# Performance work log

Hardware: AMD Instinct MI355X
Metric: run time of the kernel (lower is better)

## Reference

```python
import jax, jax.numpy as jnp
import numpy as np

B, S, D = 16, 2048, 256

def setup_inputs() -> dict:
    key = jax.random.key(0)
    ks = jax.random.split(key, 7)
    scale = 1.0 / np.sqrt(D)
    return {
        "x": jax.random.normal(ks[0], (B, S, D), dtype=jnp.float32),
        "Wq": jax.random.normal(ks[1], (D, D), dtype=jnp.float32) * scale,
        "bq": jax.random.normal(ks[2], (D,), dtype=jnp.float32) * 0.01,
        "Wk": jax.random.normal(ks[3], (D, D), dtype=jnp.float32) * scale,
        "bk": jax.random.normal(ks[4], (D,), dtype=jnp.float32) * 0.01,
        "Wv": jax.random.normal(ks[5], (D, D), dtype=jnp.float32) * scale,
        "bv": jax.random.normal(ks[6], (D,), dtype=jnp.float32) * 0.01,
    }

def reference(x, Wq, bq, Wk, bk, Wv, bv):
    # q,k,v: [B,S,D]
    q = x @ Wq + bq
    k = x @ Wk + bk
    v = x @ Wv + bv
    inv_sqrt_d = jnp.asarray(1.0 / np.sqrt(x.shape[-1]), dtype=x.dtype)
    energy = jnp.einsum('bqd,bkd->bqk', q, k) * inv_sqrt_d  # [B,S,S]
    attn = jax.nn.softmax(energy, axis=-1)
    weighted = jnp.einsum('bqk,bkd->bqd', attn, v)  # [B,S,D]
    return weighted.sum(axis=1)  # [B,D]
```

## Files before the change

kernel.cpp:

```cpp
#include <hip/hip_runtime.h>
#include <hip/hip_bf16.h>

typedef __bf16 bf16_t;
typedef bf16_t bf16x8 __attribute__((ext_vector_type(8)));
typedef float  f32x4  __attribute__((ext_vector_type(4)));

constexpr int S = 2048, D = 256;


__device__ __forceinline__ float fast_exp2(float x) {
    return __builtin_amdgcn_exp2f(x);
}

__global__ void wt_kernel(const float* __restrict__ Wq, const float* __restrict__ Wk,
                          const float* __restrict__ Wv, bf16_t* __restrict__ wtf) {
    int idx = blockIdx.x * 256 + threadIdx.x;
    int w    = idx >> 13;
    int rem  = idx & 8191;
    int nt   = rem >> 9;
    int rem2 = rem & 511;
    int ks   = rem2 >> 6;
    int lane = rem2 & 63;
    int lm = lane & 15, lg = lane >> 4;
    const float* Wsrc = (w == 0) ? Wq : (w == 1) ? Wk : Wv;
    int col = nt * 16 + lm, krow = ks * 32 + lg * 8;
    bf16x8 o;
#pragma unroll
    for (int j = 0; j < 8; j++) o[j] = (bf16_t)Wsrc[(krow + j) * 256 + col];
    *(bf16x8*)(wtf + (size_t)idx * 8) = o;
}

__global__ __launch_bounds__(256) void proj_kernel(
    const float* __restrict__ x, const bf16_t* __restrict__ wtf,
    const float* __restrict__ bq, const float* __restrict__ bk, const float* __restrict__ bv,
    bf16_t* __restrict__ qo, bf16_t* __restrict__ ko, bf16_t* __restrict__ vo) {
    __shared__ float xs[2][128 * 36];
    int w    = blockIdx.y;
    int tid  = threadIdx.x;
    int wave = tid >> 6, lane = tid & 63, lm = lane & 15, lg = lane >> 4;
    int m0   = blockIdx.x * 128;
    const bf16_t* wb   = wtf + w * 65536;
    const float*  bias = (w == 0) ? bq : (w == 1) ? bk : bv;

    f32x4 acc[2][16];
#pragma unroll
    for (int s = 0; s < 2; s++)
#pragma unroll
        for (int nt = 0; nt < 16; nt++) acc[s][nt] = f32x4{0.f, 0.f, 0.f, 0.f};

    float4 stg[4];
#pragma unroll
    for (int u = 0; u < 4; u++) {
        int f = u * 256 + tid, row = f >> 3, c4 = f & 7;
        stg[u] = *(const float4*)(x + (size_t)(m0 + row) * 256 + c4 * 4);
    }

    for (int ks = 0; ks < 8; ks++) {
        int p = ks & 1;
#pragma unroll
        for (int u = 0; u < 4; u++) {
            int f = u * 256 + tid, row = f >> 3, c4 = f & 7;
            *(float4*)&xs[p][row * 36 + c4 * 4] = stg[u];
        }
        if (ks < 7) {
#pragma unroll
            for (int u = 0; u < 4; u++) {
                int f = u * 256 + tid, row = f >> 3, c4 = f & 7;
                stg[u] = *(const float4*)(x + (size_t)(m0 + row) * 256 + (ks + 1) * 32 + c4 * 4);
            }
        }
        __syncthreads();
        bf16x8 af[2];
#pragma unroll
        for (int s = 0; s < 2; s++) {
            const float* sp = &xs[p][(wave * 32 + s * 16 + lm) * 36 + lg * 8];
            float4 h0 = *(const float4*)sp;
            float4 h1 = *(const float4*)(sp + 4);
            af[s][0] = (bf16_t)h0.x; af[s][1] = (bf16_t)h0.y;
            af[s][2] = (bf16_t)h0.z; af[s][3] = (bf16_t)h0.w;
            af[s][4] = (bf16_t)h1.x; af[s][5] = (bf16_t)h1.y;
            af[s][6] = (bf16_t)h1.z; af[s][7] = (bf16_t)h1.w;
        }
#pragma unroll
        for (int nt = 0; nt < 16; nt++) {
            bf16x8 bfr = *(const bf16x8*)(wb + (size_t)(nt * 8 + ks) * 512 + lane * 8);
            acc[0][nt] = __builtin_amdgcn_mfma_f32_16x16x32_bf16(af[0], bfr, acc[0][nt], 0, 0, 0);
            acc[1][nt] = __builtin_amdgcn_mfma_f32_16x16x32_bf16(af[1], bfr, acc[1][nt], 0, 0, 0);
        }
    }

    __syncthreads();
    bf16_t* sb = ((bf16_t*)&xs[0][0]) + wave * 4480;
    int bglob = m0 >> 11;
#pragma unroll
    for (int s = 0; s < 2; s++) {
#pragma unroll
        for (int nt = 0; nt < 16; nt++) {
            int col = nt * 16 + lm;
            float bval = bias[col];
#pragma unroll
            for (int r = 0; r < 4; r++)
                sb[(lg * 4 + r) * 280 + col] = (bf16_t)(acc[s][nt][r] + bval);
        }
        if (w == 2) {
            int ssrow = (m0 & 2047) + wave * 32 + s * 16 + lm;
#pragma unroll
            for (int ks = 0; ks < 8; ks++) {
                bf16x8 v8 = *(const bf16x8*)&sb[lm * 280 + ks * 32 + lg * 8];
                *(bf16x8*)(vo + ((size_t)(bglob * 2048 + ssrow)) * 256 + ks * 32 + lg * 8) = v8;
            }
        } else {
            bf16_t* dst = (w == 0) ? qo : ko;
            int qb = ((m0 & 2047) >> 4) + wave * 2 + s;
#pragma unroll
            for (int ks = 0; ks < 8; ks++) {
                bf16x8 v8 = *(const bf16x8*)&sb[lm * 280 + ks * 32 + lg * 8];
                *(bf16x8*)(dst + ((size_t)((bglob * 128 + qb) * 8 + ks)) * 512 + lane * 8) = v8;
            }
        }
    }
}

template <int PASS>
__global__ __launch_bounds__(512) void attn_pass(
    const bf16_t* __restrict__ q, const bf16_t* __restrict__ kmat,
    float* __restrict__ lpart, float* __restrict__ wpart) {
    __shared__ bf16_t kst[2][8192];
    __shared__ float  wacc[8][512];

    int tid  = threadIdx.x;
    int wave = tid >> 6, lane = tid & 63, lm = lane & 15, lg = lane >> 4;
    int i  = blockIdx.x;
    int b  = ((i & 7) << 1) | ((i >> 8) & 1);
    int qt = (i >> 3) & 7;
    int kh = (i >> 6) & 3;

    bf16x8 af[2][8];
#pragma unroll
    for (int s = 0; s < 2; s++) {
        const bf16_t* qb = q + ((size_t)((b * 128 + qt * 16 + wave * 2 + s) * 8)) * 512;
#pragma unroll
        for (int ks = 0; ks < 8; ks++)
            af[s][ks] = *(const bf16x8*)(qb + ks * 512 + lane * 8);
    }

    float rinv[2][4];
    if (PASS == 2) {
#pragma unroll
        for (int s = 0; s < 2; s++)
#pragma unroll
            for (int r = 0; r < 4; r++) {
                int row = qt * 256 + wave * 32 + s * 16 + lg * 4 + r;
                float l = 0.f;
#pragma unroll
                for (int k2 = 0; k2 < 4; k2++)
                    l += lpart[(size_t)(k2 * 16 + b) * 2048 + row];
                rinv[s][r] = 1.0f / l;
            }
    }

    float lsum[2][4];
#pragma unroll
    for (int s = 0; s < 2; s++)
#pragma unroll
        for (int r = 0; r < 4; r++) lsum[s][r] = 0.f;

    constexpr float SCL = 0.0625f * 1.44269504f;
    const bf16_t* kb_base = kmat + (size_t)(b * 128 + kh * 32) * 4096;

    bf16x8 stg[2];
#pragma unroll
    for (int u = 0; u < 2; u++)
        stg[u] = *(const bf16x8*)(kb_base + (size_t)(u * 512 + tid) * 8);

    for (int t = 0; t < 16; t++) {
        int p = t & 1;
#pragma unroll
        for (int u = 0; u < 2; u++)
            *(bf16x8*)&kst[p][(u * 512 + tid) * 8] = stg[u];
        if (t < 15) {
#pragma unroll
            for (int u = 0; u < 2; u++)
                stg[u] = *(const bf16x8*)(kb_base + (size_t)(t + 1) * 8192 + (u * 512 + tid) * 8);
        }
        __syncthreads();

        f32x4 sacc[2][2];
#pragma unroll
        for (int s = 0; s < 2; s++)
#pragma unroll
            for (int kb = 0; kb < 2; kb++) sacc[s][kb] = f32x4{0.f, 0.f, 0.f, 0.f};
#pragma unroll
        for (int ks = 0; ks < 8; ks++) {
#pragma unroll
            for (int kb = 0; kb < 2; kb++) {
                bf16x8 bfr = *(const bf16x8*)&kst[p][(kb * 8 + ks) * 512 + lane * 8];
                sacc[0][kb] = __builtin_amdgcn_mfma_f32_16x16x32_bf16(af[0][ks], bfr, sacc[0][kb], 0, 0, 0);
                sacc[1][kb] = __builtin_amdgcn_mfma_f32_16x16x32_bf16(af[1][ks], bfr, sacc[1][kb], 0, 0, 0);
            }
        }

        if (PASS == 1) {
#pragma unroll
            for (int s = 0; s < 2; s++)
#pragma unroll
                for (int kb = 0; kb < 2; kb++)
#pragma unroll
                    for (int r = 0; r < 4; r++)
                        lsum[s][r] += fast_exp2(sacc[s][kb][r] * SCL);
        } else {
            float wv[2] = {0.f, 0.f};
#pragma unroll
            for (int s = 0; s < 2; s++)
#pragma unroll
                for (int kb = 0; kb < 2; kb++)
#pragma unroll
                    for (int r = 0; r < 4; r++)
                        wv[kb] += fast_exp2(sacc[s][kb][r] * SCL) * rinv[s][r];
#pragma unroll
            for (int kb = 0; kb < 2; kb++) {
                float vsum = wv[kb];
                vsum += __shfl_xor(vsum, 16);
                vsum += __shfl_xor(vsum, 32);
                if (lg == 0) wacc[wave][t * 32 + kb * 16 + lm] = vsum;
            }
        }
    }

    if (PASS == 1) {
#pragma unroll
        for (int s = 0; s < 2; s++)
#pragma unroll
            for (int r = 0; r < 4; r++) {
                float v2 = lsum[s][r];
                v2 += __shfl_xor(v2, 1);
                v2 += __shfl_xor(v2, 2);
                v2 += __shfl_xor(v2, 4);
                v2 += __shfl_xor(v2, 8);
                if (lm == 0) {
                    int row = qt * 256 + wave * 32 + s * 16 + lg * 4 + r;
                    lpart[(size_t)(kh * 16 + b) * 2048 + row] = v2;
                }
            }
    } else {
        __syncthreads();
        float sum = 0.f;
#pragma unroll
        for (int w2 = 0; w2 < 8; w2++) sum += wacc[w2][tid];
        wpart[(size_t)(qt * 16 + b) * 2048 + kh * 512 + tid] = sum;
    }
}

__global__ __launch_bounds__(256) void gemv_kernel(
    const float* __restrict__ wpart, const bf16_t* __restrict__ v,
    float* __restrict__ gpart) {
    __shared__ float ldsw[256];
    int b = blockIdx.x >> 3, kseg = blockIdx.x & 7, tid = threadIdx.x;
    int key = kseg * 256 + tid;
    float s = 0.f;
#pragma unroll
    for (int qt = 0; qt < 8; qt++) s += wpart[(size_t)(qt * 16 + b) * 2048 + key];
    ldsw[tid] = s;
    __syncthreads();
    const bf16_t* vb = v + ((size_t)b * 2048 + kseg * 256) * 256;
    float acc = 0.f;
#pragma unroll 4
    for (int t = 0; t < 256; t++) acc += ldsw[t] * (float)vb[(size_t)t * 256 + tid];
    gpart[(size_t)(kseg * 16 + b) * 256 + tid] = acc;
}

__global__ void reduce_kernel(const float* __restrict__ gpart, float* __restrict__ out) {
    int b = blockIdx.x, d = threadIdx.x;
    float t = 0.f;
#pragma unroll
    for (int ks = 0; ks < 8; ks++) t += gpart[(size_t)(ks * 16 + b) * 256 + d];
    out[b * 256 + d] = t;
}

extern "C" void kernel_launch(void* const* d_in, const int* in_sizes, int n_in,
                              void* d_out, int out_size, void* d_ws, size_t ws_size,
                              hipStream_t stream) {
    const float* x  = (const float*)d_in[0];
    const float* Wq = (const float*)d_in[1];
    const float* bq = (const float*)d_in[2];
    const float* Wk = (const float*)d_in[3];
    const float* bk = (const float*)d_in[4];
    const float* Wv = (const float*)d_in[5];
    const float* bv = (const float*)d_in[6];
    float* out = (float*)d_out;

    char* ws = (char*)d_ws;
    bf16_t* wtf   = (bf16_t*)(ws);
    bf16_t* q     = (bf16_t*)(ws + 393216);
    bf16_t* kmat  = (bf16_t*)(ws + 17170432);
    bf16_t* v     = (bf16_t*)(ws + 33947648);
    float*  lpart = (float*) (ws + 50724864);
    float*  wpart = (float*) (ws + 51249152);
    float*  gpart = (float*) (ws + 52297728);

    wt_kernel<<<dim3(96), dim3(256), 0, stream>>>(Wq, Wk, Wv, wtf);
    proj_kernel<<<dim3(256, 3), dim3(256), 0, stream>>>(x, wtf, bq, bk, bv, q, kmat, v);
    attn_pass<1><<<dim3(512), dim3(512), 0, stream>>>(q, kmat, lpart, wpart);
    attn_pass<2><<<dim3(512), dim3(512), 0, stream>>>(q, kmat, lpart, wpart);
    gemv_kernel<<<dim3(128), dim3(256), 0, stream>>>(wpart, v, gpart);
    reduce_kernel<<<dim3(16), dim3(256), 0, stream>>>(gpart, out);
}
```

Baseline: 221.7 us.

## Skip V projection via associativity, reading x directly and enlarging K tiles

The V projection is eliminated by computing the attention-weighted sum of x rows per batch, then applying Wv once to that vector and adding 2048 times bv, since the softmax rows sum to one. This removes a third of the projection GEMM and the bf16 V buffer write and read. The projection kernel now loads x straight from global memory into registers instead of double-buffering through LDS with barriers. The attention kernels process 64 keys per step instead of 32 and store per-wave partials in bf16, which adds LDS use and some rounding error.

```diff
diff --git a/kernel.cpp b/kernel.cpp
--- a/kernel.cpp
+++ b/kernel.cpp
@@ -13,7 +13,7 @@
 }
 
 __global__ void wt_kernel(const float* __restrict__ Wq, const float* __restrict__ Wk,
-                          const float* __restrict__ Wv, bf16_t* __restrict__ wtf) {
+                          bf16_t* __restrict__ wtf) {
     int idx = blockIdx.x * 256 + threadIdx.x;
     int w    = idx >> 13;
     int rem  = idx & 8191;
@@ -22,7 +22,7 @@
     int ks   = rem2 >> 6;
     int lane = rem2 & 63;
     int lm = lane & 15, lg = lane >> 4;
-    const float* Wsrc = (w == 0) ? Wq : (w == 1) ? Wk : Wv;
+    const float* Wsrc = (w == 0) ? Wq : Wk;
     int col = nt * 16 + lm, krow = ks * 32 + lg * 8;
     bf16x8 o;
 #pragma unroll
@@ -32,15 +32,15 @@
 
 __global__ __launch_bounds__(256) void proj_kernel(
     const float* __restrict__ x, const bf16_t* __restrict__ wtf,
-    const float* __restrict__ bq, const float* __restrict__ bk, const float* __restrict__ bv,
-    bf16_t* __restrict__ qo, bf16_t* __restrict__ ko, bf16_t* __restrict__ vo) {
-    __shared__ float xs[2][128 * 36];
+    const float* __restrict__ bq, const float* __restrict__ bk,
+    bf16_t* __restrict__ qo, bf16_t* __restrict__ ko) {
+    __shared__ bf16_t sb_all[4][4480];
     int w    = blockIdx.y;
     int tid  = threadIdx.x;
     int wave = tid >> 6, lane = tid & 63, lm = lane & 15, lg = lane >> 4;
     int m0   = blockIdx.x * 128;
     const bf16_t* wb   = wtf + w * 65536;
-    const float*  bias = (w == 0) ? bq : (w == 1) ? bk : bv;
+    const float*  bias = (w == 0) ? bq : bk;
 
     f32x4 acc[2][16];
 #pragma unroll
@@ -48,38 +48,24 @@
 #pragma unroll
         for (int nt = 0; nt < 16; nt++) acc[s][nt] = f32x4{0.f, 0.f, 0.f, 0.f};
 
-    float4 stg[4];
-#pragma unroll
-    for (int u = 0; u < 4; u++) {
-        int f = u * 256 + tid, row = f >> 3, c4 = f & 7;
-        stg[u] = *(const float4*)(x + (size_t)(m0 + row) * 256 + c4 * 4);
-    }
+    const float* xr0 = x + (size_t)(m0 + wave * 32 + lm) * 256 + lg * 8;
+    const float* xr1 = xr0 + 16 * 256;
 
     for (int ks = 0; ks < 8; ks++) {
-        int p = ks & 1;
-#pragma unroll
-        for (int u = 0; u < 4; u++) {
-            int f = u * 256 + tid, row = f >> 3, c4 = f & 7;
-            *(float4*)&xs[p][row * 36 + c4 * 4] = stg[u];
-        }
-        if (ks < 7) {
-#pragma unroll
-            for (int u = 0; u < 4; u++) {
-                int f = u * 256 + tid, row = f >> 3, c4 = f & 7;
-                stg[u] = *(const float4*)(x + (size_t)(m0 + row) * 256 + (ks + 1) * 32 + c4 * 4);
-            }
-        }
-        __syncthreads();
         bf16x8 af[2];
-#pragma unroll
-        for (int s = 0; s < 2; s++) {
-            const float* sp = &xs[p][(wave * 32 + s * 16 + lm) * 36 + lg * 8];
-            float4 h0 = *(const float4*)sp;
-            float4 h1 = *(const float4*)(sp + 4);
-            af[s][0] = (bf16_t)h0.x; af[s][1] = (bf16_t)h0.y;
-            af[s][2] = (bf16_t)h0.z; af[s][3] = (bf16_t)h0.w;
-            af[s][4] = (bf16_t)h1.x; af[s][5] = (bf16_t)h1.y;
-            af[s][6] = (bf16_t)h1.z; af[s][7] = (bf16_t)h1.w;
+        {
+            float4 a0 = *(const float4*)(xr0 + ks * 32);
+            float4 a1 = *(const float4*)(xr0 + ks * 32 + 4);
+            float4 b0 = *(const float4*)(xr1 + ks * 32);
+            float4 b1 = *(const float4*)(xr1 + ks * 32 + 4);
+            af[0][0] = (bf16_t)a0.x; af[0][1] = (bf16_t)a0.y;
+            af[0][2] = (bf16_t)a0.z; af[0][3] = (bf16_t)a0.w;
+            af[0][4] = (bf16_t)a1.x; af[0][5] = (bf16_t)a1.y;
+            af[0][6] = (bf16_t)a1.z; af[0][7] = (bf16_t)a1.w;
+            af[1][0] = (bf16_t)b0.x; af[1][1] = (bf16_t)b0.y;
+            af[1][2] = (bf16_t)b0.z; af[1][3] = (bf16_t)b0.w;
+            af[1][4] = (bf16_t)b1.x; af[1][5] = (bf16_t)b1.y;
+            af[1][6] = (bf16_t)b1.z; af[1][7] = (bf16_t)b1.w;
         }
 #pragma unroll
         for (int nt = 0; nt < 16; nt++) {
@@ -89,9 +75,9 @@
         }
     }
 
-    __syncthreads();
-    bf16_t* sb = ((bf16_t*)&xs[0][0]) + wave * 4480;
+    bf16_t* sb = sb_all[wave];
     int bglob = m0 >> 11;
+    bf16_t* dst = (w == 0) ? qo : ko;
 #pragma unroll
     for (int s = 0; s < 2; s++) {
 #pragma unroll
@@ -102,21 +88,11 @@
             for (int r = 0; r < 4; r++)
                 sb[(lg * 4 + r) * 280 + col] = (bf16_t)(acc[s][nt][r] + bval);
         }
-        if (w == 2) {
-            int ssrow = (m0 & 2047) + wave * 32 + s * 16 + lm;
-#pragma unroll
-            for (int ks = 0; ks < 8; ks++) {
-                bf16x8 v8 = *(const bf16x8*)&sb[lm * 280 + ks * 32 + lg * 8];
-                *(bf16x8*)(vo + ((size_t)(bglob * 2048 + ssrow)) * 256 + ks * 32 + lg * 8) = v8;
-            }
-        } else {
-            bf16_t* dst = (w == 0) ? qo : ko;
-            int qb = ((m0 & 2047) >> 4) + wave * 2 + s;
-#pragma unroll
-            for (int ks = 0; ks < 8; ks++) {
-                bf16x8 v8 = *(const bf16x8*)&sb[lm * 280 + ks * 32 + lg * 8];
-                *(bf16x8*)(dst + ((size_t)((bglob * 128 + qb) * 8 + ks)) * 512 + lane * 8) = v8;
-            }
+        int qb = ((m0 & 2047) >> 4) + wave * 2 + s;
+#pragma unroll
+        for (int ks = 0; ks < 8; ks++) {
+            bf16x8 v8 = *(const bf16x8*)&sb[lm * 280 + ks * 32 + lg * 8];
+            *(bf16x8*)(dst + ((size_t)((bglob * 128 + qb) * 8 + ks)) * 512 + lane * 8) = v8;
         }
     }
 }
@@ -125,8 +101,8 @@
 __global__ __launch_bounds__(512) void attn_pass(
     const bf16_t* __restrict__ q, const bf16_t* __restrict__ kmat,
     float* __restrict__ lpart, float* __restrict__ wpart) {
-    __shared__ bf16_t kst[2][8192];
-    __shared__ float  wacc[8][512];
+    __shared__ bf16_t kst[2][16384];
+    __shared__ bf16_t wacc[8][512];
 
     int tid  = threadIdx.x;
     int wave = tid >> 6, lane = tid & 63, lm = lane & 15, lg = lane >> 4;
@@ -168,32 +144,32 @@
     constexpr float SCL = 0.0625f * 1.44269504f;
     const bf16_t* kb_base = kmat + (size_t)(b * 128 + kh * 32) * 4096;
 
-    bf16x8 stg[2];
-#pragma unroll
-    for (int u = 0; u < 2; u++)
+    bf16x8 stg[4];
+#pragma unroll
+    for (int u = 0; u < 4; u++)
         stg[u] = *(const bf16x8*)(kb_base + (size_t)(u * 512 + tid) * 8);
 
-    for (int t = 0; t < 16; t++) {
+    for (int t = 0; t < 8; t++) {
         int p = t & 1;
 #pragma unroll
-        for (int u = 0; u < 2; u++)
+        for (int u = 0; u < 4; u++)
             *(bf16x8*)&kst[p][(u * 512 + tid) * 8] = stg[u];
-        if (t < 15) {
-#pragma unroll
-            for (int u = 0; u < 2; u++)
-                stg[u] = *(const bf16x8*)(kb_base + (size_t)(t + 1) * 8192 + (u * 512 + tid) * 8);
+        if (t < 7) {
+#pragma unroll
+            for (int u = 0; u < 4; u++)
+                stg[u] = *(const bf16x8*)(kb_base + (size_t)(t + 1) * 16384 + (u * 512 + tid) * 8);
         }
         __syncthreads();
 
-        f32x4 sacc[2][2];
+        f32x4 sacc[2][4];
 #pragma unroll
         for (int s = 0; s < 2; s++)
 #pragma unroll
-            for (int kb = 0; kb < 2; kb++) sacc[s][kb] = f32x4{0.f, 0.f, 0.f, 0.f};
+            for (int kb = 0; kb < 4; kb++) sacc[s][kb] = f32x4{0.f, 0.f, 0.f, 0.f};
 #pragma unroll
         for (int ks = 0; ks < 8; ks++) {
 #pragma unroll
-            for (int kb = 0; kb < 2; kb++) {
+            for (int kb = 0; kb < 4; kb++) {
                 bf16x8 bfr = *(const bf16x8*)&kst[p][(kb * 8 + ks) * 512 + lane * 8];
                 sacc[0][kb] = __builtin_amdgcn_mfma_f32_16x16x32_bf16(af[0][ks], bfr, sacc[0][kb], 0, 0, 0);
                 sacc[1][kb] = __builtin_amdgcn_mfma_f32_16x16x32_bf16(af[1][ks], bfr, sacc[1][kb], 0, 0, 0);
@@ -204,25 +180,25 @@
 #pragma unroll
             for (int s = 0; s < 2; s++)
 #pragma unroll
-                for (int kb = 0; kb < 2; kb++)
+                for (int kb = 0; kb < 4; kb++)
 #pragma unroll
                     for (int r = 0; r < 4; r++)
                         lsum[s][r] += fast_exp2(sacc[s][kb][r] * SCL);
         } else {
-            float wv[2] = {0.f, 0.f};
+            float wv[4] = {0.f, 0.f, 0.f, 0.f};
 #pragma unroll
             for (int s = 0; s < 2; s++)
 #pragma unroll
-                for (int kb = 0; kb < 2; kb++)
+                for (int kb = 0; kb < 4; kb++)
 #pragma unroll
                     for (int r = 0; r < 4; r++)
                         wv[kb] += fast_exp2(sacc[s][kb][r] * SCL) * rinv[s][r];
 #pragma unroll
-            for (int kb = 0; kb < 2; kb++) {
+            for (int kb = 0; kb < 4; kb++) {
                 float vsum = wv[kb];
                 vsum += __shfl_xor(vsum, 16);
                 vsum += __shfl_xor(vsum, 32);
-                if (lg == 0) wacc[wave][t * 32 + kb * 16 + lm] = vsum;
+                if (lg == 0) wacc[wave][t * 64 + kb * 16 + lm] = (bf16_t)vsum;
             }
         }
     }
@@ -246,35 +222,45 @@
         __syncthreads();
         float sum = 0.f;
 #pragma unroll
-        for (int w2 = 0; w2 < 8; w2++) sum += wacc[w2][tid];
+        for (int w2 = 0; w2 < 8; w2++) sum += (float)wacc[w2][tid];
         wpart[(size_t)(qt * 16 + b) * 2048 + kh * 512 + tid] = sum;
     }
 }
 
-__global__ __launch_bounds__(256) void gemv_kernel(
-    const float* __restrict__ wpart, const bf16_t* __restrict__ v,
+__global__ __launch_bounds__(256) void xsum_kernel(
+    const float* __restrict__ wpart, const float* __restrict__ x,
     float* __restrict__ gpart) {
-    __shared__ float ldsw[256];
-    int b = blockIdx.x >> 3, kseg = blockIdx.x & 7, tid = threadIdx.x;
-    int key = kseg * 256 + tid;
+    __shared__ float ldsw[128];
+    int b = blockIdx.x >> 4, kseg = blockIdx.x & 15, tid = threadIdx.x;
+    if (tid < 128) {
+        int key = kseg * 128 + tid;
+        float s = 0.f;
+#pragma unroll
+        for (int qt = 0; qt < 8; qt++) s += wpart[(size_t)(qt * 16 + b) * 2048 + key];
+        ldsw[tid] = s;
+    }
+    __syncthreads();
+    const float* xb = x + ((size_t)b * 2048 + kseg * 128) * 256;
+    float acc = 0.f;
+#pragma unroll 8
+    for (int t = 0; t < 128; t++) acc += ldsw[t] * xb[(size_t)t * 256 + tid];
+    gpart[(size_t)(kseg * 16 + b) * 256 + tid] = acc;
+}
+
+__global__ __launch_bounds__(256) void final_kernel(
+    const float* __restrict__ gpart, const float* __restrict__ Wv,
+    const float* __restrict__ bv, float* __restrict__ out) {
+    __shared__ float yl[256];
+    int b = blockIdx.x, tid = threadIdx.x;
     float s = 0.f;
 #pragma unroll
-    for (int qt = 0; qt < 8; qt++) s += wpart[(size_t)(qt * 16 + b) * 2048 + key];
-    ldsw[tid] = s;
+    for (int ks = 0; ks < 16; ks++) s += gpart[(size_t)(ks * 16 + b) * 256 + tid];
+    yl[tid] = s;
     __syncthreads();
-    const bf16_t* vb = v + ((size_t)b * 2048 + kseg * 256) * 256;
     float acc = 0.f;
 #pragma unroll 4
-    for (int t = 0; t < 256; t++) acc += ldsw[t] * (float)vb[(size_t)t * 256 + tid];
-    gpart[(size_t)(kseg * 16 + b) * 256 + tid] = acc;
-}
-
-__global__ void reduce_kernel(const float* __restrict__ gpart, float* __restrict__ out) {
-    int b = blockIdx.x, d = threadIdx.x;
-    float t = 0.f;
-#pragma unroll
-    for (int ks = 0; ks < 8; ks++) t += gpart[(size_t)(ks * 16 + b) * 256 + d];
-    out[b * 256 + d] = t;
+    for (int c = 0; c < 256; c++) acc += yl[c] * Wv[c * 256 + tid];
+    out[b * 256 + tid] = acc + 2048.0f * bv[tid];
 }
 
 extern "C" void kernel_launch(void* const* d_in, const int* in_sizes, int n_in,
@@ -291,17 +277,16 @@
 
     char* ws = (char*)d_ws;
     bf16_t* wtf   = (bf16_t*)(ws);
-    bf16_t* q     = (bf16_t*)(ws + 393216);
-    bf16_t* kmat  = (bf16_t*)(ws + 17170432);
-    bf16_t* v     = (bf16_t*)(ws + 33947648);
-    float*  lpart = (float*) (ws + 50724864);
-    float*  wpart = (float*) (ws + 51249152);
-    float*  gpart = (float*) (ws + 52297728);
-
-    wt_kernel<<<dim3(96), dim3(256), 0, stream>>>(Wq, Wk, Wv, wtf);
-    proj_kernel<<<dim3(256, 3), dim3(256), 0, stream>>>(x, wtf, bq, bk, bv, q, kmat, v);
+    bf16_t* q     = (bf16_t*)(ws + 262144);
+    bf16_t* kmat  = (bf16_t*)(ws + 17039360);
+    float*  lpart = (float*) (ws + 33816576);
+    float*  wpart = (float*) (ws + 34340864);
+    float*  gpart = (float*) (ws + 35389440);
+
+    wt_kernel<<<dim3(64), dim3(256), 0, stream>>>(Wq, Wk, wtf);
+    proj_kernel<<<dim3(256, 2), dim3(256), 0, stream>>>(x, wtf, bq, bk, q, kmat);
     attn_pass<1><<<dim3(512), dim3(512), 0, stream>>>(q, kmat, lpart, wpart);
     attn_pass<2><<<dim3(512), dim3(512), 0, stream>>>(q, kmat, lpart, wpart);
-    gemv_kernel<<<dim3(128), dim3(256), 0, stream>>>(wpart, v, gpart);
-    reduce_kernel<<<dim3(16), dim3(256), 0, stream>>>(gpart, out);
-}
+    xsum_kernel<<<dim3(256), dim3(256), 0, stream>>>(wpart, x, gpart);
+    final_kernel<<<dim3(16), dim3(256), 0, stream>>>(gpart, Wv, bv, out);
+}
```

Measured after the change: 199.6 us. 10.0% less time.
